# Performance work log

Hardware: AMD Instinct MI355X
Metric: run time of the kernel (lower is better)

## Reference

```python
import jax, jax.numpy as jnp
import numpy as np

B, S1, S2 = 32, 128, 128
V, D, P, C = 30000, 300, 200, 3


def _highway(x, Wh, bh, Wt, bt):
    h = jax.nn.relu(x @ Wh + bh)
    t = jax.nn.sigmoid(x @ Wt + bt)
    return t * h + (1.0 - t) * x


def _ff(x, W1, b1, W2, b2):
    # self.forward: two relu linear layers (dropout disabled / keep_prob=1)
    return jax.nn.relu(jax.nn.relu(x @ W1 + b1) @ W2 + b2)


def setup_inputs() -> dict:
    key = jax.random.key(0)
    ks = iter(jax.random.split(key, 64))
    W = lambda *s: jax.random.normal(next(ks), s, jnp.float32) * 0.05
    Z = lambda n: jnp.zeros((n,), jnp.float32)
    inp = {
        'x1': jax.random.randint(next(ks), (B, S1), 0, V),
        'x2': jax.random.randint(next(ks), (B, S2), 0, V),
        'emb': jax.random.normal(next(ks), (V, D), jnp.float32),
        'hw1_Wh': W(D, D), 'hw1_bh': Z(D), 'hw1_Wt': W(D, D), 'hw1_bt': Z(D),
        'hw2_Wh': W(D, D), 'hw2_bh': Z(D), 'hw2_Wt': W(D, D), 'hw2_bt': Z(D),
        'mul_W1': W(D, P), 'mul_b1': Z(P), 'mul_W2': W(P, P), 'mul_b2': Z(P),
        'dist_W1': W(D, P), 'dist_b1': Z(P), 'dist_W2': W(P, P), 'dist_b2': Z(P),
        'cmp_W1': W(4 * D, P), 'cmp_b1': Z(P), 'cmp_W2': W(P, P), 'cmp_b2': Z(P),
        'chw1_Wh': W(P, P), 'chw1_bh': Z(P), 'chw1_Wt': W(P, P), 'chw1_bt': Z(P),
        'chw2_Wh': W(P, P), 'chw2_bh': Z(P), 'chw2_Wt': W(P, P), 'chw2_bt': Z(P),
        'agg_W1': W(4 * P, P), 'agg_b1': Z(P), 'agg_W2': W(P, P), 'agg_b2': Z(P),
        'out_W': W(P, C), 'out_b': Z(C),
    }
    return inp


def reference(x1, x2, emb,
              hw1_Wh, hw1_bh, hw1_Wt, hw1_bt,
              hw2_Wh, hw2_bh, hw2_Wt, hw2_bt,
              mul_W1, mul_b1, mul_W2, mul_b2,
              dist_W1, dist_b1, dist_W2, dist_b2,
              cmp_W1, cmp_b1, cmp_W2, cmp_b2,
              chw1_Wh, chw1_bh, chw1_Wt, chw1_bt,
              chw2_Wh, chw2_bh, chw2_Wt, chw2_bt,
              agg_W1, agg_b1, agg_W2, agg_b2,
              out_W, out_b):
    # embed + shared highway stack
    e1 = emb[x1]  # [B,S1,D]
    e2 = emb[x2]  # [B,S2,D]
    e1 = _highway(_highway(e1, hw1_Wh, hw1_bh, hw1_Wt, hw1_bt), hw2_Wh, hw2_bh, hw2_Wt, hw2_bt)
    e2 = _highway(_highway(e2, hw1_Wh, hw1_bh, hw1_Wt, hw1_bt), hw2_Wh, hw2_bh, hw2_Wt, hw2_bt)

    # attention_mul: project both, dot product
    p1 = _ff(e1, mul_W1, mul_b1, mul_W2, mul_b2)  # [B,S1,P]
    p2 = _ff(e2, mul_W1, mul_b1, mul_W2, mul_b2)  # [B,S2,P]
    att1 = jnp.einsum('bip,bjp->bij', p1, p2)

    # attention_dist: project both, sum_d 1/(1+|q1-q2|) -> 4D broadcast
    q1 = _ff(e1, dist_W1, dist_b1, dist_W2, dist_b2)
    q2 = _ff(e2, dist_W1, dist_b1, dist_W2, dist_b2)
    att2 = jnp.sum(1.0 / (1.0 + jnp.abs(q1[:, :, None, :] - q2[:, None, :, :])), axis=-1)

    sim = att1 + att2  # [B,S1,S2]
    alpha = jnp.einsum('bji,bjd->bid', jax.nn.softmax(jnp.swapaxes(sim, 1, 2), axis=-1).transpose(0, 2, 1).transpose(0, 2, 1), e1) if False else jnp.matmul(jax.nn.softmax(jnp.swapaxes(sim, 1, 2), axis=-1), e1)  # [B,S2,D]
    beta = jnp.matmul(jax.nn.softmax(sim, axis=-1), e2)  # [B,S1,D]

    # compare (shared forward + highway stack)
    v1 = _ff(jnp.concatenate([e1, beta, e1 - beta, e1 * beta], -1), cmp_W1, cmp_b1, cmp_W2, cmp_b2)
    v2 = _ff(jnp.concatenate([e2, alpha, e2 - alpha, e2 * alpha], -1), cmp_W1, cmp_b1, cmp_W2, cmp_b2)
    v1 = _highway(_highway(v1, chw1_Wh, chw1_bh, chw1_Wt, chw1_bt), chw2_Wh, chw2_bh, chw2_Wt, chw2_bt)
    v2 = _highway(_highway(v2, chw1_Wh, chw1_bh, chw1_Wt, chw1_bt), chw2_Wh, chw2_bh, chw2_Wt, chw2_bt)

    # aggregate: max + sum pooling, forward, final linear
    v = jnp.concatenate([v1.max(1), v2.max(1), v1.sum(1), v2.sum(1)], -1)  # [B,4P]
    y = _ff(v, agg_W1, agg_b1, agg_W2, agg_b2)
    return y @ out_W + out_b  # [B,C]
```

## Files before the change

### kernel.cpp

```cpp
#include <hip/hip_runtime.h>
#include <hip/hip_bf16.h>
#include <math.h>

#define B_   32
#define S_   128
#define V_   30000
#define D_   300
#define P_   200
#define NT   8192
#define NT1  4096
#define LDE  320
#define LDP  256

typedef __hip_bfloat16 bf16;
typedef __attribute__((ext_vector_type(8))) __bf16 bf16x8;
typedef __attribute__((ext_vector_type(4))) float f32x4;

__device__ __forceinline__ float b2f(bf16 v) { return __bfloat162float(v); }
__device__ __forceinline__ short f2s(float v) { bf16 h = __float2bfloat16(v); return *(short*)&h; }
__device__ __forceinline__ float s2f(short s) { bf16 h; *(short*)&h = s; return __bfloat162float(h); }

struct ConvTable {
    const float* W1[8]; const float* W2[8]; bf16* dst[8];
    int K[8], N1[8], N2[8], Kpad[8], IL[8];
    unsigned long long base[8]; unsigned long long total;
};

__global__ void k_convw(ConvTable T) {
    unsigned long long idx = (unsigned long long)blockIdx.x * 256 + threadIdx.x;
    if (idx >= T.total) return;
    int e = 0;
#pragma unroll
    for (int i = 1; i < 8; ++i) if (idx >= T.base[i]) e = i;
    unsigned long long local = idx - T.base[e];
    int Kpad = T.Kpad[e];
    int n = (int)(local / Kpad);
    int k = (int)(local - (unsigned long long)n * Kpad);
    float v = 0.f;
    if (k < T.K[e]) {
        if (T.IL[e]) {
            int d = n >> 1, half = n & 1;
            if (d < T.N1[e]) v = (half ? T.W2[e] : T.W1[e])[(size_t)k * T.N1[e] + d];
        } else {
            if (n < T.N1[e]) v = T.W1[e][(size_t)k * T.N1[e] + n];
            else if (n < T.N1[e] + T.N2[e]) v = T.W2[e][(size_t)k * T.N2[e] + (n - T.N1[e])];
        }
    }
    T.dst[e][local] = __float2bfloat16(v);
}

__global__ void k_convmisc(const float* __restrict__ Wc, bf16* __restrict__ dstc,
                           const float* __restrict__ A1w, const float* __restrict__ A2w,
                           const float* __restrict__ Ow,
                           float* __restrict__ T1, float* __restrict__ T2,
                           float* __restrict__ T3) {
    int idx = blockIdx.x * 256 + threadIdx.x;
    if (idx < 245760) {
        int n = idx / 960, k = idx - n * 960;
        int sel = k / 320, kc = k - sel * 320;
        float v = 0.f;
        if (kc < 300 && n < 200) {
            if (sel == 0)      v = Wc[(size_t)kc * 200 + n] + Wc[(size_t)(600 + kc) * 200 + n];
            else if (sel == 1) v = Wc[(size_t)(300 + kc) * 200 + n] - Wc[(size_t)(600 + kc) * 200 + n];
            else               v = Wc[(size_t)(900 + kc) * 200 + n];
        }
        dstc[idx] = __float2bfloat16(v);
    } else {
        int l = idx - 245760;
        if (l < 160000)       T1[l] = A1w[(size_t)(l % 800) * 200 + l / 800];
        else if (l < 200000)  { int m = l - 160000; T2[m] = A2w[(size_t)(m % 200) * 200 + m / 200]; }
        else if (l < 200600)  { int m = l - 200000; T3[m] = Ow[(size_t)(m % 200) * 3 + m / 200]; }
    }
}

__global__ __launch_bounds__(256) void k_skinny(
    const float* __restrict__ A, const float* __restrict__ WT,
    const float* __restrict__ bias, float* __restrict__ C,
    int M, int N, int K, int act) {
    int wave = (blockIdx.x * 256 + threadIdx.x) >> 6;
    int lane = threadIdx.x & 63;
    if (wave >= M * N) return;
    int m = wave / N, n = wave - m * N;
    const float4* a4 = (const float4*)(A + (size_t)m * K);
    const float4* w4 = (const float4*)(WT + (size_t)n * K);
    int K4 = K >> 2;
    float acc = 0.f;
    for (int i = lane; i < K4; i += 64) {
        float4 av = a4[i], wv = w4[i];
        acc += av.x * wv.x + av.y * wv.y + av.z * wv.z + av.w * wv.w;
    }
#pragma unroll
    for (int off = 32; off > 0; off >>= 1) acc += __shfl_down(acc, off, 64);
    if (lane == 0) {
        float v = acc + bias[n];
        if (act == 1) v = fmaxf(v, 0.f);
        C[(size_t)m * N + n] = v;
    }
}

#define TKP 40

template <int AMODE, int EPI>
__global__ __launch_bounds__(256) void k_gemm(
    const bf16* __restrict__ A, const bf16* __restrict__ A2,
    const bf16* __restrict__ A3, int lda,
    const int* __restrict__ tok1, const int* __restrict__ tok2,
    const float* __restrict__ emb,
    const bf16* __restrict__ WT, const bf16* __restrict__ WT2, int Kpad, int K,
    bf16* __restrict__ C, bf16* __restrict__ C2, int ldc, int Ntot, int N1,
    const float* __restrict__ bias1, const float* __restrict__ bias2,
    int act1, int act2, const bf16* __restrict__ xbuf, int ldxb)
{
    __shared__ short As[64][TKP];
    __shared__ short Bs[64][TKP];
    __shared__ short Cs[64][72];
    int tid = threadIdx.x;
    int w = tid >> 6, lane = tid & 63, quad = lane >> 4, l16 = lane & 15;
    int bm = blockIdx.x * 64;
    int half = 0, bn;
    if (AMODE == 4) { half = blockIdx.y >> 2; bn = (blockIdx.y & 3) * 64; }
    else bn = blockIdx.y * 64;
    const short* Wsh = (const short*)((AMODE == 4 && half) ? WT2 : WT);
    bf16* Cl = (AMODE == 4 && half) ? C2 : C;
    int wr = (w & 1) * 32, wc = (w >> 1) * 32;
    int ar = tid >> 2, ac = (tid & 3) * 8;

    const short* Abase = (const short*)A + (AMODE == 4 ? half * 200 : 0);
    int gm = bm + ar;
    int tok = 0;
    if (AMODE == 1) {
        tok = (gm < NT1) ? tok1[gm] : tok2[gm - NT1];
        if ((unsigned)tok >= (unsigned)V_) tok = 0;
    }

    f32x4 acc[2][2];
#pragma unroll
    for (int i = 0; i < 2; ++i)
#pragma unroll
        for (int j = 0; j < 2; ++j)
#pragma unroll
            for (int r = 0; r < 4; ++r) acc[i][j][r] = 0.f;

    short pa[8], pb[8];

    auto loadA = [&](int k0) {
        if (AMODE == 0 || AMODE == 4) {
            int k = k0 + ac;
            const short* src = Abase + (size_t)gm * lda + k;
            if (k + 8 <= K) {
                *(short4*)&pa[0] = ((const short4*)src)[0];
                *(short4*)&pa[4] = ((const short4*)src)[1];
            } else {
#pragma unroll
                for (int i = 0; i < 8; ++i) pa[i] = (k + i < K) ? src[i] : (short)0;
            }
        } else if (AMODE == 1) {
            int k = k0 + ac;
            const float* src = emb + (size_t)tok * 300 + k;
            float f[8];
            if (k + 8 <= K) {
                *(float4*)&f[0] = ((const float4*)src)[0];
                *(float4*)&f[4] = ((const float4*)src)[1];
            } else {
#pragma unroll
                for (int i = 0; i < 8; ++i) f[i] = (k + i < K) ? src[i] : 0.f;
            }
#pragma unroll
            for (int i = 0; i < 8; ++i) pa[i] = f2s(f[i]);
        } else {
            int sel = k0 / 320;
            const short* base = (sel == 0) ? (const short*)A
                              : (sel == 1) ? (const short*)A2 : (const short*)A3;
            int k = (k0 - sel * 320) + ac;
            const short* src = base + (size_t)gm * LDE + k;
            if (k + 8 <= 300) {
                *(short4*)&pa[0] = ((const short4*)src)[0];
                *(short4*)&pa[4] = ((const short4*)src)[1];
            } else {
#pragma unroll
                for (int i = 0; i < 8; ++i) pa[i] = (k + i < 300) ? src[i] : (short)0;
            }
        }
    };
    auto loadB = [&](int k0) {
        const short* src = Wsh + (size_t)(bn + ar) * Kpad + k0 + ac;
        *(short4*)&pb[0] = ((const short4*)src)[0];
        *(short4*)&pb[4] = ((const short4*)src)[1];
    };

    loadA(0); loadB(0);
    for (int k0 = 0; k0 < Kpad; k0 += 32) {
        *(short4*)&As[ar][ac] = *(short4*)&pa[0];
        *(short4*)&As[ar][ac + 4] = *(short4*)&pa[4];
        *(short4*)&Bs[ar][ac] = *(short4*)&pb[0];
        *(short4*)&Bs[ar][ac + 4] = *(short4*)&pb[4];
        __syncthreads();
        if (k0 + 32 < Kpad) { loadA(k0 + 32); loadB(k0 + 32); }
        {
            bf16x8 a[2], b[2];
#pragma unroll
            for (int mt = 0; mt < 2; ++mt)
                a[mt] = *(const bf16x8*)&As[wr + mt * 16 + l16][quad * 8];
#pragma unroll
            for (int nt = 0; nt < 2; ++nt)
                b[nt] = *(const bf16x8*)&Bs[wc + nt * 16 + l16][quad * 8];
#pragma unroll
            for (int mt = 0; mt < 2; ++mt)
#pragma unroll
                for (int nt = 0; nt < 2; ++nt)
                    acc[mt][nt] = __builtin_amdgcn_mfma_f32_16x16x32_bf16(a[mt], b[nt], acc[mt][nt], 0, 0, 0);
        }
        __syncthreads();
    }
#pragma unroll
    for (int mt = 0; mt < 2; ++mt) {
#pragma unroll
        for (int nt = 0; nt < 2; ++nt) {
            int cl = wc + nt * 16 + l16;
            int col = bn + cl;
            float bv; int act;
            if (EPI == 1) {
                int d = col >> 1;
                if (d > N1 - 1) d = N1 - 1;
                if (col & 1) { bv = bias2[d]; act = 2; }
                else         { bv = bias1[d]; act = 1; }
            } else if (AMODE == 4) {
                int cc = (col < N1) ? col : (N1 - 1);
                bv = (half ? bias2 : bias1)[cc]; act = act1;
            } else {
                int cc = (col < Ntot) ? col : (Ntot - 1);
                if (cc < N1) { bv = bias1[cc]; act = act1; }
                else { bv = bias2[cc - N1]; act = act2; }
            }
#pragma unroll
            for (int r = 0; r < 4; ++r) {
                float v = acc[mt][nt][r] + bv;
                if (act == 1) v = fmaxf(v, 0.f);
                else if (act == 2) v = 1.f / (1.f + expf(-v));
                Cs[wr + mt * 16 + quad * 4 + r][cl] = f2s(v);
            }
        }
    }
    __syncthreads();
    if (EPI == 0) {
#pragma unroll
        for (int it = 0; it < 2; ++it) {
            int chunk = tid + it * 256;
            int rl = chunk >> 3;
            int c8 = (chunk & 7) * 8;
            short* dst = (short*)Cl + (size_t)(bm + rl) * ldc + bn + c8;
            *(short4*)dst = *(short4*)&Cs[rl][c8];
            *(short4*)(dst + 4) = *(short4*)&Cs[rl][c8 + 4];
        }
    } else {
        int d0 = bn >> 1;
#pragma unroll
        for (int it = 0; it < 2; ++it) {
            int chunk = tid + it * 256;
            int rl = chunk >> 3;
            int c4 = (chunk & 7) * 4;
            int row = bm + rl;
            float x[4];
            if (AMODE == 1) {
                int tk = (row < NT1) ? tok1[row] : tok2[row - NT1];
                if ((unsigned)tk >= (unsigned)V_) tk = 0;
                const float* xs = emb + (size_t)tk * 300 + d0 + c4;
#pragma unroll
                for (int i = 0; i < 4; ++i) x[i] = (d0 + c4 + i < N1) ? xs[i] : 0.f;
            } else {
                const short* xs = (const short*)xbuf + (size_t)row * ldxb + d0 + c4;
#pragma unroll
                for (int i = 0; i < 4; ++i) x[i] = s2f(xs[i]);
            }
            short o[4];
#pragma unroll
            for (int i = 0; i < 4; ++i) {
                float h = s2f(Cs[rl][2 * (c4 + i)]);
                float t = s2f(Cs[rl][2 * (c4 + i) + 1]);
                o[i] = f2s(t * h + (1.f - t) * x[i]);
            }
            *(short4*)((short*)Cl + (size_t)row * ldc + d0 + c4) = *(short4*)&o[0];
        }
    }
}

__global__ void k_transpose2(const bf16* __restrict__ srcP, bf16* __restrict__ dstP,
                             const bf16* __restrict__ srcQ, bf16* __restrict__ dstQ) {
    int idx = blockIdx.x * 256 + threadIdx.x;
    if (idx >= B_ * P_ * S_) return;
    const bf16* src = blockIdx.y ? srcQ : srcP;
    bf16* dst = blockIdx.y ? dstQ : dstP;
    int j = idx & (S_ - 1);
    int rest = idx >> 7;
    int p = rest % P_;
    int b = rest / P_;
    dst[idx] = src[((size_t)(b * S_ + j)) * LDP + p];
}

__global__ __launch_bounds__(256) void k_sim2(const bf16* __restrict__ Pmat,
                                              const bf16* __restrict__ Qmat,
                                              const bf16* __restrict__ PT,
                                              const bf16* __restrict__ QT,
                                              float* __restrict__ SIM) {
    __shared__ float qp[8][P_][2];
    int blk = blockIdx.x;
    int b = blk >> 4;
    int it = blk & 15;
    int tid = threadIdx.x;
    int j = tid & 127, h = tid >> 7;
    int row0 = b * 128 + it * 8;
    for (int x = tid; x < 8 * P_; x += 256) {
        int r = x / P_, c = x - r * P_;
        qp[r][c][0] = b2f(Qmat[(size_t)(row0 + r) * LDP + c]);
        qp[r][c][1] = b2f(Pmat[(size_t)(row0 + r) * LDP + c]);
    }
    __syncthreads();
    const bf16* ptb = PT + (size_t)b * P_ * S_;
    const bf16* qtb = QT + (size_t)b * P_ * S_;
    float acc[4] = {0.f, 0.f, 0.f, 0.f};
    for (int p = 0; p < P_; ++p) {
        float v = b2f(ptb[p * S_ + j]);
        float u = b2f(qtb[p * S_ + j]);
#pragma unroll
        for (int r = 0; r < 4; ++r) {
            int i = h * 4 + r;
            float2 w = *(const float2*)&qp[i][p][0];
            float d = w.x - u;
            acc[r] += w.y * v + __builtin_amdgcn_rcpf(1.f + fabsf(d));
        }
    }
#pragma unroll
    for (int r = 0; r < 4; ++r) {
        int i = it * 8 + h * 4 + r;
        SIM[((size_t)(b * 128 + i)) * S_ + j] = acc[r];
    }
}

__global__ __launch_bounds__(256) void k_av2(const float* __restrict__ SIM,
                                             const bf16* __restrict__ E,
                                             bf16* __restrict__ OUT,
                                             bf16* __restrict__ EA) {
    int blk = blockIdx.x;
    int kind = blk >> 12;
    int blk2 = blk & 4095;
    int b = blk2 >> 7, r = blk2 & 127;
    int t = threadIdx.x;
    __shared__ float w[S_];
    __shared__ float red[S_];
    float x = 0.f;
    if (t < 128) {
        x = (kind == 0) ? SIM[(size_t)blk2 * S_ + t]
                        : SIM[((size_t)b * S_ + t) * S_ + r];
        red[t] = x;
    }
    __syncthreads();
    for (int s = 64; s > 0; s >>= 1) {
        if (t < s) red[t] = fmaxf(red[t], red[t + s]);
        __syncthreads();
    }
    float mx = red[0];
    __syncthreads();
    float ex = 0.f;
    if (t < 128) { ex = expf(x - mx); red[t] = ex; }
    __syncthreads();
    for (int s = 64; s > 0; s >>= 1) {
        if (t < s) red[t] += red[t + s];
        __syncthreads();
    }
    if (t < 128) w[t] = ex / red[0];
    __syncthreads();
    if (t < 150) {
        int orow_idx = (kind == 0) ? blk2 : (NT1 + blk2);
        const bf16* Esrc = E + (kind == 0 ? (size_t)NT1 * LDE : 0) + (size_t)b * S_ * LDE;
        const unsigned short* ebase = (const unsigned short*)Esrc + 2 * t;
        float a0 = 0.f, a1 = 0.f;
        for (int s = 0; s < S_; ++s) {
            unsigned int uv = *(const unsigned int*)(ebase + (size_t)s * LDE);
            float lo = __uint_as_float(uv << 16);
            float hi = __uint_as_float(uv & 0xffff0000u);
            float ws = w[s];
            a0 += ws * lo;
            a1 += ws * hi;
        }
        unsigned int o = (unsigned int)(unsigned short)f2s(a0)
                       | ((unsigned int)(unsigned short)f2s(a1) << 16);
        *(unsigned int*)((unsigned short*)OUT + (size_t)orow_idx * LDE + 2 * t) = o;
        unsigned int ev = *(const unsigned int*)((const unsigned short*)E + (size_t)orow_idx * LDE + 2 * t);
        float e0 = __uint_as_float(ev << 16);
        float e1 = __uint_as_float(ev & 0xffff0000u);
        unsigned int o2 = (unsigned int)(unsigned short)f2s(a0 * e0)
                        | ((unsigned int)(unsigned short)f2s(a1 * e1) << 16);
        *(unsigned int*)((unsigned short*)EA + (size_t)orow_idx * LDE + 2 * t) = o2;
    }
}

__global__ __launch_bounds__(256) void k_pool(const bf16* __restrict__ V,
                                              float* __restrict__ OUT) {
    int b = blockIdx.x;
    int c = threadIdx.x;
    if (c >= P_) return;
    const bf16* v1 = V + (size_t)(b * S_) * LDP;
    const bf16* v2 = V + (size_t)(NT1 + b * S_) * LDP;
    float mx1 = -INFINITY, mx2 = -INFINITY, s1 = 0.f, s2 = 0.f;
    for (int i = 0; i < S_; ++i) {
        float a = b2f(v1[(size_t)i * LDP + c]);
        mx1 = fmaxf(mx1, a); s1 += a;
        float bb = b2f(v2[(size_t)i * LDP + c]);
        mx2 = fmaxf(mx2, bb); s2 += bb;
    }
    float* o = OUT + (size_t)b * 4 * P_;
    o[c] = mx1; o[P_ + c] = mx2; o[2 * P_ + c] = s1; o[3 * P_ + c] = s2;
}

__global__ void k_fillf(float* dst, int n, float v) {
    int i = blockIdx.x * 256 + threadIdx.x;
    if (i < n) dst[i] = v;
}

extern "C" void kernel_launch(void* const* d_in, const int* in_sizes, int n_in,
                              void* d_out, int out_size, void* d_ws, size_t ws_size,
                              hipStream_t stream) {
    const int* x1 = (const int*)d_in[0];
    const int* x2 = (const int*)d_in[1];
    const float* emb = (const float*)d_in[2];
    const float *hw1_Wh = (const float*)d_in[3],  *hw1_bh = (const float*)d_in[4];
    const float *hw1_Wt = (const float*)d_in[5],  *hw1_bt = (const float*)d_in[6];
    const float *hw2_Wh = (const float*)d_in[7],  *hw2_bh = (const float*)d_in[8];
    const float *hw2_Wt = (const float*)d_in[9],  *hw2_bt = (const float*)d_in[10];
    const float *mul_W1 = (const float*)d_in[11], *mul_b1 = (const float*)d_in[12];
    const float *mul_W2 = (const float*)d_in[13], *mul_b2 = (const float*)d_in[14];
    const float *dist_W1 = (const float*)d_in[15], *dist_b1 = (const float*)d_in[16];
    const float *dist_W2 = (const float*)d_in[17], *dist_b2 = (const float*)d_in[18];
    const float *cmp_W1 = (const float*)d_in[19], *cmp_b1 = (const float*)d_in[20];
    const float *cmp_W2 = (const float*)d_in[21], *cmp_b2 = (const float*)d_in[22];
    const float *chw1_Wh = (const float*)d_in[23], *chw1_bh = (const float*)d_in[24];
    const float *chw1_Wt = (const float*)d_in[25], *chw1_bt = (const float*)d_in[26];
    const float *chw2_Wh = (const float*)d_in[27], *chw2_bh = (const float*)d_in[28];
    const float *chw2_Wt = (const float*)d_in[29], *chw2_bt = (const float*)d_in[30];
    const float *agg_W1 = (const float*)d_in[31], *agg_b1 = (const float*)d_in[32];
    const float *agg_W2 = (const float*)d_in[33], *agg_b2 = (const float*)d_in[34];
    const float *out_W = (const float*)d_in[35], *out_b = (const float*)d_in[36];

    const size_t nE = (size_t)NT * LDE;
    const size_t nP = (size_t)NT * LDP;
    const size_t nCht = (size_t)NT * 448;
    const size_t nTR = (size_t)B_ * P_ * S_;
    const size_t nWT = 1171456;
    size_t bf16_elems = 4 * nE + 2 * nP + 2 * nCht + nWT;
    size_t f32_elems = (size_t)B_ * 4 * P_ + 2 * (size_t)B_ * P_ + 200600;
    size_t need = bf16_elems * 2 + f32_elems * 4 + 64;
    if (ws_size < need) {
        k_fillf<<<dim3(1), dim3(256), 0, stream>>>((float*)d_out, B_ * 3, 555.f);
        return;
    }
    bf16* X1  = (bf16*)d_ws;
    bf16* X2  = X1 + nE;
    bf16* ATT = X2 + nE;
    bf16* EA  = ATT + nE;
    bf16* Pb  = EA + nE;
    bf16* Qb  = Pb + nP;
    bf16* ChtA = Qb + nP;
    bf16* ChtB = ChtA + nCht;
    bf16* WTp = ChtB + nCht;
    float* POOL = (float*)(WTp + nWT);
    float* G1 = POOL + (size_t)B_ * 4 * P_;
    float* G2 = G1 + (size_t)B_ * P_;
    float* WT_a1 = G2 + (size_t)B_ * P_;
    float* WT_a2 = WT_a1 + 160000;
    float* WT_o  = WT_a2 + 40000;
    bf16* PTb = ChtB;
    bf16* QTb = ChtB + nTR;
    float* SIM = (float*)(ChtB + 2 * nTR);
    bf16* V2 = ChtB;

    bf16* WT_hw1 = WTp + 0;
    bf16* WT_hw2 = WTp + 204800;
    bf16* WT_md  = WTp + 409600;
    bf16* WT_m2  = WTp + 552960;
    bf16* WT_d2  = WTp + 610304;
    bf16* WT_c2  = WTp + 667648;
    bf16* WT_ch1 = WTp + 724992;
    bf16* WT_ch2 = WTp + 825344;
    bf16* WT_c1  = WTp + 925696;

    dim3 blk256(256);

    ConvTable T;
    const float* s1[8] = {hw1_Wh, hw2_Wh, mul_W1, mul_W2, dist_W2, cmp_W2, chw1_Wh, chw2_Wh};
    const float* s2[8] = {hw1_Wt, hw2_Wt, dist_W1, nullptr, nullptr, nullptr, chw1_Wt, chw2_Wt};
    bf16* dsts[8] = {WT_hw1, WT_hw2, WT_md, WT_m2, WT_d2, WT_c2, WT_ch1, WT_ch2};
    int Ks[8]  = {300, 300, 300, 200, 200, 200, 200, 200};
    int N1s[8] = {300, 300, 200, 200, 200, 200, 200, 200};
    int N2s[8] = {300, 300, 200, 0, 0, 0, 200, 200};
    int Kps[8] = {320, 320, 320, 224, 224, 224, 224, 224};
    int Nps[8] = {640, 640, 448, 256, 256, 256, 448, 448};
    int ILs[8] = {1, 1, 0, 0, 0, 0, 1, 1};
    unsigned long long base = 0;
    for (int i = 0; i < 8; ++i) {
        T.W1[i] = s1[i]; T.W2[i] = s2[i]; T.dst[i] = dsts[i];
        T.K[i] = Ks[i]; T.N1[i] = N1s[i]; T.N2[i] = N2s[i]; T.Kpad[i] = Kps[i];
        T.IL[i] = ILs[i];
        T.base[i] = base;
        base += (unsigned long long)Kps[i] * Nps[i];
    }
    T.total = base;
    k_convw<<<dim3((unsigned)((base + 255) / 256)), blk256, 0, stream>>>(T);
    k_convmisc<<<dim3((245760 + 200600 + 255) / 256), blk256, 0, stream>>>(
        cmp_W1, WT_c1, agg_W1, agg_W2, out_W, WT_a1, WT_a2, WT_o);

    k_gemm<1, 1><<<dim3(128, 10), blk256, 0, stream>>>(
        nullptr, nullptr, nullptr, 0, x1, x2, emb,
        WT_hw1, nullptr, 320, 300, X1, nullptr, LDE, 600, 300,
        hw1_bh, hw1_bt, 1, 2, nullptr, 0);

    k_gemm<0, 1><<<dim3(128, 10), blk256, 0, stream>>>(
        X1, nullptr, nullptr, LDE, nullptr, nullptr, nullptr,
        WT_hw2, nullptr, 320, 300, X2, nullptr, LDE, 600, 300,
        hw2_bh, hw2_bt, 1, 2, X1, LDE);

    k_gemm<0, 0><<<dim3(128, 7), blk256, 0, stream>>>(
        X2, nullptr, nullptr, LDE, nullptr, nullptr, nullptr,
        WT_md, nullptr, 320, 300, ChtA, nullptr, 448, 400, 200,
        mul_b1, dist_b1, 1, 1, nullptr, 0);

    k_gemm<4, 0><<<dim3(128, 8), blk256, 0, stream>>>(
        ChtA, nullptr, nullptr, 448, nullptr, nullptr, nullptr,
        WT_m2, WT_d2, 224, 200, Pb, Qb, LDP, 256, 200,
        mul_b2, dist_b2, 1, 1, nullptr, 0);

    int nTRb = (int)((nTR + 255) / 256);
    k_transpose2<<<dim3(nTRb, 2), blk256, 0, stream>>>(
        Pb + (size_t)NT1 * LDP, PTb, Qb + (size_t)NT1 * LDP, QTb);

    k_sim2<<<dim3(B_ * 16), blk256, 0, stream>>>(Pb, Qb, PTb, QTb, SIM);

    k_av2<<<dim3(2 * NT1), blk256, 0, stream>>>(SIM, X2, ATT, EA);

    k_gemm<3, 0><<<dim3(128, 4), blk256, 0, stream>>>(
        X2, ATT, EA, LDE, nullptr, nullptr, nullptr,
        WT_c1, nullptr, 960, 300, ChtA, nullptr, LDP, 256, 200,
        cmp_b1, cmp_b1, 1, 1, nullptr, 0);

    k_gemm<0, 0><<<dim3(128, 4), blk256, 0, stream>>>(
        ChtA, nullptr, nullptr, LDP, nullptr, nullptr, nullptr,
        WT_c2, nullptr, 224, 200, Pb, nullptr, LDP, 256, 200,
        cmp_b2, cmp_b2, 1, 1, nullptr, 0);

    k_gemm<0, 1><<<dim3(128, 7), blk256, 0, stream>>>(
        Pb, nullptr, nullptr, LDP, nullptr, nullptr, nullptr,
        WT_ch1, nullptr, 224, 200, Qb, nullptr, LDP, 400, 200,
        chw1_bh, chw1_bt, 1, 2, Pb, LDP);

    k_gemm<0, 1><<<dim3(128, 7), blk256, 0, stream>>>(
        Qb, nullptr, nullptr, LDP, nullptr, nullptr, nullptr,
        WT_ch2, nullptr, 224, 200, V2, nullptr, LDP, 400, 200,
        chw2_bh, chw2_bt, 1, 2, Qb, LDP);

    k_pool<<<dim3(B_), blk256, 0, stream>>>(V2, POOL);

    k_skinny<<<dim3(1600), blk256, 0, stream>>>(POOL, WT_a1, agg_b1, G1, B_, P_, 800, 1);
    k_skinny<<<dim3(1600), blk256, 0, stream>>>(G1, WT_a2, agg_b2, G2, B_, P_, 200, 1);
    k_skinny<<<dim3(24), blk256, 0, stream>>>(G2, WT_o, out_b, (float*)d_out, B_, 3, 200, 0);
}
```

Measured before the change: 367.0 us.

## Deepen GEMM K-tile to 64, pre-gather embeddings into bf16 buffer

The GEMM kernel now steps K by 64 instead of 32 and issues two MFMAs per fragment, which halves the number of barrier pairs per tile, and the epilogue staging buffer reuses the A tile's shared memory. Embedding rows are gathered and converted to bf16 by a separate kernel, so the first highway GEMM reads a dense bf16 matrix instead of doing gathers and fp32 conversion inside its load loop. To fit the 64-wide K step, the weights for the 200-wide layers are padded to K=256, which adds zero-padded work. The extra embed kernel adds one launch and one extra round trip through memory.

```diff
diff --git a/kernel.cpp b/kernel.cpp
--- a/kernel.cpp
+++ b/kernel.cpp
@@ -71,6 +71,28 @@
         else if (l < 200000)  { int m = l - 160000; T2[m] = A2w[(size_t)(m % 200) * 200 + m / 200]; }
         else if (l < 200600)  { int m = l - 200000; T3[m] = Ow[(size_t)(m % 200) * 3 + m / 200]; }
     }
+}
+
+__global__ void k_embed(const int* __restrict__ x1, const int* __restrict__ x2,
+                        const float* __restrict__ emb, bf16* __restrict__ E) {
+    int idx = blockIdx.x * 256 + threadIdx.x;
+    if (idx >= NT * (LDE / 4)) return;
+    int r = idx / (LDE / 4);
+    int c4 = (idx - r * (LDE / 4)) * 4;
+    int tok = (r < NT1) ? x1[r] : x2[r - NT1];
+    if ((unsigned)tok >= (unsigned)V_) tok = 0;
+    short o[4];
+    if (c4 + 4 <= 300) {
+        float4 v = *(const float4*)(emb + (size_t)tok * 300 + c4);
+        o[0] = f2s(v.x); o[1] = f2s(v.y); o[2] = f2s(v.z); o[3] = f2s(v.w);
+    } else {
+#pragma unroll
+        for (int i = 0; i < 4; ++i) {
+            int c = c4 + i;
+            o[i] = f2s((c < 300) ? emb[(size_t)tok * 300 + c] : 0.f);
+        }
+    }
+    *(short4*)((short*)E + (size_t)r * LDE + c4) = *(short4*)&o[0];
 }
 
 __global__ __launch_bounds__(256) void k_skinny(
@@ -98,22 +120,17 @@
     }
 }
 
-#define TKP 40
-
 template <int AMODE, int EPI>
 __global__ __launch_bounds__(256) void k_gemm(
     const bf16* __restrict__ A, const bf16* __restrict__ A2,
     const bf16* __restrict__ A3, int lda,
-    const int* __restrict__ tok1, const int* __restrict__ tok2,
-    const float* __restrict__ emb,
     const bf16* __restrict__ WT, const bf16* __restrict__ WT2, int Kpad, int K,
     bf16* __restrict__ C, bf16* __restrict__ C2, int ldc, int Ntot, int N1,
     const float* __restrict__ bias1, const float* __restrict__ bias2,
     int act1, int act2, const bf16* __restrict__ xbuf, int ldxb)
 {
-    __shared__ short As[64][TKP];
-    __shared__ short Bs[64][TKP];
-    __shared__ short Cs[64][72];
+    __shared__ short As[64][72];
+    __shared__ short Bs[64][72];
     int tid = threadIdx.x;
     int w = tid >> 6, lane = tid & 63, quad = lane >> 4, l16 = lane & 15;
     int bm = blockIdx.x * 64;
@@ -123,15 +140,10 @@
     const short* Wsh = (const short*)((AMODE == 4 && half) ? WT2 : WT);
     bf16* Cl = (AMODE == 4 && half) ? C2 : C;
     int wr = (w & 1) * 32, wc = (w >> 1) * 32;
-    int ar = tid >> 2, ac = (tid & 3) * 8;
+    int ar = tid >> 2, ac = (tid & 3) * 16;
 
     const short* Abase = (const short*)A + (AMODE == 4 ? half * 200 : 0);
     int gm = bm + ar;
-    int tok = 0;
-    if (AMODE == 1) {
-        tok = (gm < NT1) ? tok1[gm] : tok2[gm - NT1];
-        if ((unsigned)tok >= (unsigned)V_) tok = 0;
-    }
 
     f32x4 acc[2][2];
 #pragma unroll
@@ -141,77 +153,72 @@
 #pragma unroll
             for (int r = 0; r < 4; ++r) acc[i][j][r] = 0.f;
 
-    short pa[8], pb[8];
+    short pa[16], pb[16];
 
     auto loadA = [&](int k0) {
-        if (AMODE == 0 || AMODE == 4) {
+        if (AMODE != 3) {
             int k = k0 + ac;
             const short* src = Abase + (size_t)gm * lda + k;
-            if (k + 8 <= K) {
-                *(short4*)&pa[0] = ((const short4*)src)[0];
-                *(short4*)&pa[4] = ((const short4*)src)[1];
+            if (k + 16 <= K) {
+#pragma unroll
+                for (int i = 0; i < 4; ++i) *(short4*)&pa[i * 4] = ((const short4*)src)[i];
             } else {
 #pragma unroll
-                for (int i = 0; i < 8; ++i) pa[i] = (k + i < K) ? src[i] : (short)0;
+                for (int i = 0; i < 16; ++i) pa[i] = (k + i < K) ? src[i] : (short)0;
             }
-        } else if (AMODE == 1) {
-            int k = k0 + ac;
-            const float* src = emb + (size_t)tok * 300 + k;
-            float f[8];
-            if (k + 8 <= K) {
-                *(float4*)&f[0] = ((const float4*)src)[0];
-                *(float4*)&f[4] = ((const float4*)src)[1];
-            } else {
-#pragma unroll
-                for (int i = 0; i < 8; ++i) f[i] = (k + i < K) ? src[i] : 0.f;
-            }
-#pragma unroll
-            for (int i = 0; i < 8; ++i) pa[i] = f2s(f[i]);
         } else {
             int sel = k0 / 320;
             const short* base = (sel == 0) ? (const short*)A
                               : (sel == 1) ? (const short*)A2 : (const short*)A3;
             int k = (k0 - sel * 320) + ac;
             const short* src = base + (size_t)gm * LDE + k;
-            if (k + 8 <= 300) {
-                *(short4*)&pa[0] = ((const short4*)src)[0];
-                *(short4*)&pa[4] = ((const short4*)src)[1];
+            if (k + 16 <= 300) {
+#pragma unroll
+                for (int i = 0; i < 4; ++i) *(short4*)&pa[i * 4] = ((const short4*)src)[i];
             } else {
 #pragma unroll
-                for (int i = 0; i < 8; ++i) pa[i] = (k + i < 300) ? src[i] : (short)0;
+                for (int i = 0; i < 16; ++i) pa[i] = (k + i < 300) ? src[i] : (short)0;
             }
         }
     };
     auto loadB = [&](int k0) {
         const short* src = Wsh + (size_t)(bn + ar) * Kpad + k0 + ac;
-        *(short4*)&pb[0] = ((const short4*)src)[0];
-        *(short4*)&pb[4] = ((const short4*)src)[1];
+#pragma unroll
+        for (int i = 0; i < 4; ++i) *(short4*)&pb[i * 4] = ((const short4*)src)[i];
     };
 
     loadA(0); loadB(0);
-    for (int k0 = 0; k0 < Kpad; k0 += 32) {
-        *(short4*)&As[ar][ac] = *(short4*)&pa[0];
-        *(short4*)&As[ar][ac + 4] = *(short4*)&pa[4];
-        *(short4*)&Bs[ar][ac] = *(short4*)&pb[0];
-        *(short4*)&Bs[ar][ac + 4] = *(short4*)&pb[4];
+    for (int k0 = 0; k0 < Kpad; k0 += 64) {
+#pragma unroll
+        for (int i = 0; i < 4; ++i) {
+            *(short4*)&As[ar][ac + i * 4] = *(short4*)&pa[i * 4];
+            *(short4*)&Bs[ar][ac + i * 4] = *(short4*)&pb[i * 4];
+        }
         __syncthreads();
-        if (k0 + 32 < Kpad) { loadA(k0 + 32); loadB(k0 + 32); }
+        if (k0 + 64 < Kpad) { loadA(k0 + 64); loadB(k0 + 64); }
         {
-            bf16x8 a[2], b[2];
+            bf16x8 a[2][2], b[2][2];
 #pragma unroll
             for (int mt = 0; mt < 2; ++mt)
-                a[mt] = *(const bf16x8*)&As[wr + mt * 16 + l16][quad * 8];
+#pragma unroll
+                for (int ks = 0; ks < 2; ++ks)
+                    a[mt][ks] = *(const bf16x8*)&As[wr + mt * 16 + l16][ks * 32 + quad * 8];
 #pragma unroll
             for (int nt = 0; nt < 2; ++nt)
-                b[nt] = *(const bf16x8*)&Bs[wc + nt * 16 + l16][quad * 8];
+#pragma unroll
+                for (int ks = 0; ks < 2; ++ks)
+                    b[nt][ks] = *(const bf16x8*)&Bs[wc + nt * 16 + l16][ks * 32 + quad * 8];
 #pragma unroll
             for (int mt = 0; mt < 2; ++mt)
 #pragma unroll
-                for (int nt = 0; nt < 2; ++nt)
-                    acc[mt][nt] = __builtin_amdgcn_mfma_f32_16x16x32_bf16(a[mt], b[nt], acc[mt][nt], 0, 0, 0);
+                for (int nt = 0; nt < 2; ++nt) {
+                    acc[mt][nt] = __builtin_amdgcn_mfma_f32_16x16x32_bf16(a[mt][0], b[nt][0], acc[mt][nt], 0, 0, 0);
+                    acc[mt][nt] = __builtin_amdgcn_mfma_f32_16x16x32_bf16(a[mt][1], b[nt][1], acc[mt][nt], 0, 0, 0);
+                }
         }
         __syncthreads();
     }
+    short (*Cs)[72] = As;
 #pragma unroll
     for (int mt = 0; mt < 2; ++mt) {
 #pragma unroll
@@ -260,24 +267,13 @@
             int rl = chunk >> 3;
             int c4 = (chunk & 7) * 4;
             int row = bm + rl;
-            float x[4];
-            if (AMODE == 1) {
-                int tk = (row < NT1) ? tok1[row] : tok2[row - NT1];
-                if ((unsigned)tk >= (unsigned)V_) tk = 0;
-                const float* xs = emb + (size_t)tk * 300 + d0 + c4;
-#pragma unroll
-                for (int i = 0; i < 4; ++i) x[i] = (d0 + c4 + i < N1) ? xs[i] : 0.f;
-            } else {
-                const short* xs = (const short*)xbuf + (size_t)row * ldxb + d0 + c4;
-#pragma unroll
-                for (int i = 0; i < 4; ++i) x[i] = s2f(xs[i]);
-            }
+            const short* xs = (const short*)xbuf + (size_t)row * ldxb + d0 + c4;
             short o[4];
 #pragma unroll
             for (int i = 0; i < 4; ++i) {
                 float h = s2f(Cs[rl][2 * (c4 + i)]);
                 float t = s2f(Cs[rl][2 * (c4 + i) + 1]);
-                o[i] = f2s(t * h + (1.f - t) * x[i]);
+                o[i] = f2s(t * h + (1.f - t) * s2f(xs[i]));
             }
             *(short4*)((short*)Cl + (size_t)row * ldc + d0 + c4) = *(short4*)&o[0];
         }
@@ -445,7 +441,7 @@
     const size_t nP = (size_t)NT * LDP;
     const size_t nCht = (size_t)NT * 448;
     const size_t nTR = (size_t)B_ * P_ * S_;
-    const size_t nWT = 1171456;
+    const size_t nWT = 1224704;
     size_t bf16_elems = 4 * nE + 2 * nP + 2 * nCht + nWT;
     size_t f32_elems = (size_t)B_ * 4 * P_ + 2 * (size_t)B_ * P_ + 200600;
     size_t need = bf16_elems * 2 + f32_elems * 4 + 64;
@@ -453,10 +449,10 @@
         k_fillf<<<dim3(1), dim3(256), 0, stream>>>((float*)d_out, B_ * 3, 555.f);
         return;
     }
-    bf16* X1  = (bf16*)d_ws;
+    bf16* Eb  = (bf16*)d_ws;
+    bf16* X1  = Eb + nE;
     bf16* X2  = X1 + nE;
-    bf16* ATT = X2 + nE;
-    bf16* EA  = ATT + nE;
+    bf16* EA  = X2 + nE;
     bf16* Pb  = EA + nE;
     bf16* Qb  = Pb + nP;
     bf16* ChtA = Qb + nP;
@@ -468,6 +464,7 @@
     float* WT_a1 = G2 + (size_t)B_ * P_;
     float* WT_a2 = WT_a1 + 160000;
     float* WT_o  = WT_a2 + 40000;
+    bf16* ATT = Eb;
     bf16* PTb = ChtB;
     bf16* QTb = ChtB + nTR;
     float* SIM = (float*)(ChtB + 2 * nTR);
@@ -477,11 +474,11 @@
     bf16* WT_hw2 = WTp + 204800;
     bf16* WT_md  = WTp + 409600;
     bf16* WT_m2  = WTp + 552960;
-    bf16* WT_d2  = WTp + 610304;
-    bf16* WT_c2  = WTp + 667648;
-    bf16* WT_ch1 = WTp + 724992;
-    bf16* WT_ch2 = WTp + 825344;
-    bf16* WT_c1  = WTp + 925696;
+    bf16* WT_d2  = WTp + 618496;
+    bf16* WT_c2  = WTp + 684032;
+    bf16* WT_ch1 = WTp + 749568;
+    bf16* WT_ch2 = WTp + 864256;
+    bf16* WT_c1  = WTp + 978944;
 
     dim3 blk256(256);
 
@@ -492,7 +489,7 @@
     int Ks[8]  = {300, 300, 300, 200, 200, 200, 200, 200};
     int N1s[8] = {300, 300, 200, 200, 200, 200, 200, 200};
     int N2s[8] = {300, 300, 200, 0, 0, 0, 200, 200};
-    int Kps[8] = {320, 320, 320, 224, 224, 224, 224, 224};
+    int Kps[8] = {320, 320, 320, 256, 256, 256, 256, 256};
     int Nps[8] = {640, 640, 448, 256, 256, 256, 448, 448};
     int ILs[8] = {1, 1, 0, 0, 0, 0, 1, 1};
     unsigned long long base = 0;
@@ -508,24 +505,26 @@
     k_convmisc<<<dim3((245760 + 200600 + 255) / 256), blk256, 0, stream>>>(
         cmp_W1, WT_c1, agg_W1, agg_W2, out_W, WT_a1, WT_a2, WT_o);
 
-    k_gemm<1, 1><<<dim3(128, 10), blk256, 0, stream>>>(
-        nullptr, nullptr, nullptr, 0, x1, x2, emb,
+    k_embed<<<dim3((NT * (LDE / 4) + 255) / 256), blk256, 0, stream>>>(x1, x2, emb, Eb);
+
+    k_gemm<0, 1><<<dim3(128, 10), blk256, 0, stream>>>(
+        Eb, nullptr, nullptr, LDE,
         WT_hw1, nullptr, 320, 300, X1, nullptr, LDE, 600, 300,
-        hw1_bh, hw1_bt, 1, 2, nullptr, 0);
+        hw1_bh, hw1_bt, 1, 2, Eb, LDE);
 
     k_gemm<0, 1><<<dim3(128, 10), blk256, 0, stream>>>(
-        X1, nullptr, nullptr, LDE, nullptr, nullptr, nullptr,
+        X1, nullptr, nullptr, LDE,
         WT_hw2, nullptr, 320, 300, X2, nullptr, LDE, 600, 300,
         hw2_bh, hw2_bt, 1, 2, X1, LDE);
 
     k_gemm<0, 0><<<dim3(128, 7), blk256, 0, stream>>>(
-        X2, nullptr, nullptr, LDE, nullptr, nullptr, nullptr,
+        X2, nullptr, nullptr, LDE,
         WT_md, nullptr, 320, 300, ChtA, nullptr, 448, 400, 200,
         mul_b1, dist_b1, 1, 1, nullptr, 0);
 
     k_gemm<4, 0><<<dim3(128, 8), blk256, 0, stream>>>(
-        ChtA, nullptr, nullptr, 448, nullptr, nullptr, nullptr,
-        WT_m2, WT_d2, 224, 200, Pb, Qb, LDP, 256, 200,
+        ChtA, nullptr, nullptr, 448,
+        WT_m2, WT_d2, 256, 200, Pb, Qb, LDP, 256, 200,
         mul_b2, dist_b2, 1, 1, nullptr, 0);
 
     int nTRb = (int)((nTR + 255) / 256);
@@ -537,23 +536,23 @@
     k_av2<<<dim3(2 * NT1), blk256, 0, stream>>>(SIM, X2, ATT, EA);
 
     k_gemm<3, 0><<<dim3(128, 4), blk256, 0, stream>>>(
-        X2, ATT, EA, LDE, nullptr, nullptr, nullptr,
-        WT_c1, nullptr, 960, 300, ChtA, nullptr, LDP, 256, 200,
+        X2, ATT, EA, LDE,
+        WT_c1, nullptr, 960, 300, ChtA, nullptr, LDP, 200, 200,
         cmp_b1, cmp_b1, 1, 1, nullptr, 0);
 
     k_gemm<0, 0><<<dim3(128, 4), blk256, 0, stream>>>(
-        ChtA, nullptr, nullptr, LDP, nullptr, nullptr, nullptr,
-        WT_c2, nullptr, 224, 200, Pb, nullptr, LDP, 256, 200,
+        ChtA, nullptr, nullptr, LDP,
+        WT_c2, nullptr, 256, 200, Pb, nullptr, LDP, 200, 200,
         cmp_b2, cmp_b2, 1, 1, nullptr, 0);
 
     k_gemm<0, 1><<<dim3(128, 7), blk256, 0, stream>>>(
-        Pb, nullptr, nullptr, LDP, nullptr, nullptr, nullptr,
-        WT_ch1, nullptr, 224, 200, Qb, nullptr, LDP, 400, 200,
+        Pb, nullptr, nullptr, LDP,
+        WT_ch1, nullptr, 256, 200, Qb, nullptr, LDP, 400, 200,
         chw1_bh, chw1_bt, 1, 2, Pb, LDP);
 
     k_gemm<0, 1><<<dim3(128, 7), blk256, 0, stream>>>(
-        Qb, nullptr, nullptr, LDP, nullptr, nullptr, nullptr,
-        WT_ch2, nullptr, 224, 200, V2, nullptr, LDP, 400, 200,
+        Qb, nullptr, nullptr, LDP,
+        WT_ch2, nullptr, 256, 200, V2, nullptr, LDP, 400, 200,
         chw2_bh, chw2_bt, 1, 2, Qb, LDP);
 
     k_pool<<<dim3(B_), blk256, 0, stream>>>(V2, POOL);
```

Measured after the change: 337.2 us. 1.09x faster.
